# Kernel tuning notes

Hardware: AMD Instinct MI355X
Metric: run time of the kernel (lower is better)

The kernel has to match this reference:

```python
import jax, jax.numpy as jnp
import numpy as np
import math

B, S, E, H = 4, 1024, 1024, 16
D = E // H


def setup_inputs() -> dict:
    key = jax.random.key(0)
    ks = jax.random.split(key, 10)
    inp = {
        "query": jax.random.normal(ks[0], (B, S, E), dtype=jnp.float32),
        "key": jax.random.normal(ks[1], (B, S, E), dtype=jnp.float32),
        "value": jax.random.normal(ks[2], (B, S, E), dtype=jnp.float32),
        "attn_mask": jax.random.randint(ks[3], (B * H, S, S), 0, 2).astype(bool),
        "key_padding_mask": jax.random.randint(ks[4], (B, S), 0, 2).astype(bool),
        # nn.Linear(E, E, bias=False) weights, stored [out, in] as in torch
        "Wq": jax.random.normal(ks[5], (E, E), dtype=jnp.float32) * 0.02,
        "Wk": jax.random.normal(ks[6], (E, E), dtype=jnp.float32) * 0.02,
        "Wv": jax.random.normal(ks[7], (E, E), dtype=jnp.float32) * 0.02,
        "Wo": jax.random.normal(ks[8], (E, E), dtype=jnp.float32) * 0.02,
    }
    return inp


def reference(query, key, value, attn_mask, key_padding_mask, Wq, Wk, Wv, Wo):
    # projections: torch Linear => x @ W.T; split heads -> [B,H,S,D]
    Q = (query @ Wq.T).reshape(B, S, H, D).transpose(0, 2, 1, 3)
    K = (key @ Wk.T).reshape(B, S, H, D).transpose(0, 2, 1, 3)
    V = (value @ Wv.T).reshape(B, S, H, D).transpose(0, 2, 1, 3)

    scores = jnp.einsum('bhid,bhkd->bhik', Q, K) / math.sqrt(D)  # [B,H,S,S]

    am = attn_mask.reshape(B, H, S, S)
    kpm = jnp.broadcast_to(key_padding_mask[:, None, None, :], (B, H, S, S))
    mask = am | kpm

    # faithful quirks: masked scores set to 0 (not -inf); softmax over dim=2
    # (the QUERY axis i of [b,h,i,k]); masked weights zeroed after softmax.
    scores = jnp.where(mask, 0.0, scores)
    weights = jax.nn.softmax(scores, axis=2)
    weights = jnp.where(mask, 0.0, weights)

    attn = jnp.einsum('bhij,bhjk->bhik', weights, V)  # [B,H,S,D]
    attn = attn.transpose(0, 2, 1, 3).reshape(B, S, H * D)
    return attn @ Wo.T
```

## Files before the change

### kernel.cpp

```cpp
#include <hip/hip_runtime.h>
#include <stdint.h>

#define S_ 1024
#define E_ 1024
#define H_ 16
#define D_ 64
#define BH_ 64

typedef __attribute__((ext_vector_type(4))) float f32x4;
typedef __attribute__((ext_vector_type(8))) short bf16x8;

__device__ __forceinline__ ushort f2bf(float f) {
  union { float f; uint32_t u; } c; c.f = f;
  uint32_t u = c.u;
  return (ushort)((u + 0x7FFFu + ((u >> 16) & 1u)) >> 16);
}

__device__ __forceinline__ void gl_lds16(const void* g, void* l) {
  __builtin_amdgcn_global_load_lds((__attribute__((address_space(1))) void*)(g),
                                   (__attribute__((address_space(3))) void*)(l), 16, 0, 0);
}

__global__ __launch_bounds__(256) void cvt_bf16(const float* __restrict__ q,
                                                const float* __restrict__ k,
                                                const float* __restrict__ v,
                                                const float* __restrict__ wq,
                                                const float* __restrict__ wk,
                                                const float* __restrict__ wv,
                                                const float* __restrict__ wo,
                                                ushort* __restrict__ dst) {
  size_t i = ((size_t)blockIdx.x * 256 + threadIdx.x) * 4;
  const size_t M4 = 4u << 20, M1 = 1u << 20;
  const float* src;
  size_t off;
  if (i < M4) { src = q; off = i; }
  else if (i < 2 * M4) { src = k; off = i - M4; }
  else if (i < 3 * M4) { src = v; off = i - 2 * M4; }
  else if (i < 3 * M4 + M1) { src = wq; off = i - 3 * M4; }
  else if (i < 3 * M4 + 2 * M1) { src = wk; off = i - (3 * M4 + M1); }
  else if (i < 3 * M4 + 3 * M1) { src = wv; off = i - (3 * M4 + 2 * M1); }
  else { src = wo; off = i - (3 * M4 + 3 * M1); }
  float4 f = *reinterpret_cast<const float4*>(src + off);
  ushort4 o;
  o.x = f2bf(f.x); o.y = f2bf(f.y); o.z = f2bf(f.z); o.w = f2bf(f.w);
  *reinterpret_cast<ushort4*>(dst + i) = o;
}

__global__ __launch_bounds__(256) void pack_mask(const int* __restrict__ am,
                                                 const int* __restrict__ kpm,
                                                 uint32_t* __restrict__ mw) {
  size_t t = (size_t)blockIdx.x * 256 + threadIdx.x;
  size_t f = t * 4;
  int k = (int)(f & (S_ - 1));
  int b = (int)(f >> 24);
  int4 a = *reinterpret_cast<const int4*>(am + f);
  int4 kp = *reinterpret_cast<const int4*>(kpm + (size_t)b * S_ + k);
  uint32_t nib = (uint32_t)((a.x | kp.x) != 0) | ((uint32_t)((a.y | kp.y) != 0) << 1) |
                 ((uint32_t)((a.z | kp.z) != 0) << 2) | ((uint32_t)((a.w | kp.w) != 0) << 3);
  uint32_t v = nib << ((threadIdx.x & 7) * 4);
  v |= __shfl_xor(v, 1);
  v |= __shfl_xor(v, 2);
  v |= __shfl_xor(v, 4);
  if ((threadIdx.x & 7) == 0) mw[t >> 3] = v;
}

__global__ __launch_bounds__(256) void gemm_proj(const ushort* __restrict__ qkv,
                                                 const ushort* __restrict__ wts,
                                                 ushort* __restrict__ QKo,
                                                 ushort* __restrict__ Vt) {
  const int K = 1024, BM = 128, BK = 32;
  __shared__ ushort As[BM * BK];
  __shared__ ushort Bs[BM * BK];
  const int tid = threadIdx.x, wave = tid >> 6, lane = tid & 63;
  const int l15 = lane & 15, lk = lane >> 4;
  const int wr = wave >> 1, wc = wave & 1;
  const int mb = blockIdx.x, nb = blockIdx.y, z = blockIdx.z;
  const ushort* A = qkv + (size_t)z * (4u << 20);
  const ushort* Bw = wts + (size_t)z * (1u << 20);
  const int srow = (lane >> 2);
  const int scol = (lane & 3) * 8;
  f32x4 acc[4][4] = {};
  for (int kt = 0; kt < K / BK; ++kt) {
#pragma unroll
    for (int c = 0; c < 2; ++c) {
      int ch = wave * 2 + c;
      int row = ch * 16 + srow;
      gl_lds16(&A[(size_t)(mb * BM + row) * K + kt * BK + scol], &As[ch * 512]);
      gl_lds16(&Bw[(size_t)(nb * BM + row) * K + kt * BK + scol], &Bs[ch * 512]);
    }
    __syncthreads();
    bf16x8 a[4], b[4];
#pragma unroll
    for (int m = 0; m < 4; ++m)
      a[m] = *reinterpret_cast<const bf16x8*>(&As[(wr * 64 + m * 16 + l15) * BK + lk * 8]);
#pragma unroll
    for (int n = 0; n < 4; ++n)
      b[n] = *reinterpret_cast<const bf16x8*>(&Bs[(wc * 64 + n * 16 + l15) * BK + lk * 8]);
#pragma unroll
    for (int m = 0; m < 4; ++m)
#pragma unroll
      for (int n = 0; n < 4; ++n)
        acc[m][n] = __builtin_amdgcn_mfma_f32_16x16x32_bf16(a[m], b[n], acc[m][n], 0, 0, 0);
    __syncthreads();
  }
#pragma unroll
  for (int m = 0; m < 4; ++m) {
#pragma unroll
    for (int n = 0; n < 4; ++n) {
#pragma unroll
      for (int r = 0; r < 4; ++r) {
        int gm = mb * BM + wr * 64 + m * 16 + lk * 4 + r;
        int gn = nb * BM + wc * 64 + n * 16 + l15;
        int bb = gm >> 10, s = gm & 1023, h = gn >> 6, d = gn & 63;
        int bh = bb * 16 + h;
        ushort v = f2bf(acc[m][n][r]);
        if (z == 2)
          Vt[((size_t)bh * D_ + d) * S_ + s] = v;
        else
          QKo[(size_t)z * (4u << 20) + ((size_t)bh * S_ + s) * D_ + d] = v;
      }
    }
  }
}

__global__ __launch_bounds__(256) void gemm_out(const ushort* __restrict__ An,
                                                const ushort* __restrict__ Bw,
                                                float* __restrict__ outp) {
  const int K = 1024, BM = 128, BN = 64, BK = 32;
  __shared__ ushort As[BM * BK];
  __shared__ ushort Bs[BN * BK];
  const int tid = threadIdx.x, wave = tid >> 6, lane = tid & 63;
  const int l15 = lane & 15, lk = lane >> 4;
  const int wr = wave >> 1, wc = wave & 1;
  const int mb = blockIdx.x, nb = blockIdx.y;
  const int srow = (lane >> 2), scol = (lane & 3) * 8;
  f32x4 acc[4][2] = {};
  for (int kt = 0; kt < K / BK; ++kt) {
#pragma unroll
    for (int c = 0; c < 2; ++c) {
      int ch = wave * 2 + c;
      int row = ch * 16 + srow;
      gl_lds16(&An[(size_t)(mb * BM + row) * K + kt * BK + scol], &As[ch * 512]);
    }
    {
      int row = wave * 16 + srow;
      gl_lds16(&Bw[(size_t)(nb * BN + row) * K + kt * BK + scol], &Bs[wave * 512]);
    }
    __syncthreads();
    bf16x8 a[4], b[2];
#pragma unroll
    for (int m = 0; m < 4; ++m)
      a[m] = *reinterpret_cast<const bf16x8*>(&As[(wr * 64 + m * 16 + l15) * BK + lk * 8]);
#pragma unroll
    for (int n = 0; n < 2; ++n)
      b[n] = *reinterpret_cast<const bf16x8*>(&Bs[(wc * 32 + n * 16 + l15) * BK + lk * 8]);
#pragma unroll
    for (int m = 0; m < 4; ++m)
#pragma unroll
      for (int n = 0; n < 2; ++n)
        acc[m][n] = __builtin_amdgcn_mfma_f32_16x16x32_bf16(a[m], b[n], acc[m][n], 0, 0, 0);
    __syncthreads();
  }
#pragma unroll
  for (int m = 0; m < 4; ++m) {
#pragma unroll
    for (int n = 0; n < 2; ++n) {
#pragma unroll
      for (int r = 0; r < 4; ++r) {
        int gm = mb * BM + wr * 64 + m * 16 + lk * 4 + r;
        int gn = nb * BN + wc * 32 + n * 16 + l15;
        outp[(size_t)gm * 1024 + gn] = acc[m][n][r];
      }
    }
  }
}

__global__ __launch_bounds__(256) void attn_pass_a(const ushort* __restrict__ Qh,
                                                   const ushort* __restrict__ Kh,
                                                   const uint32_t* __restrict__ mw,
                                                   float* __restrict__ denom) {
  const int TI = 128, TK = 128, LD = 72;
  __shared__ ushort Qs[TI * LD];
  __shared__ ushort Ks[TK * LD];
  __shared__ uint32_t Ms[TI * 4];
  __shared__ float red[4][64];
  const int tid = threadIdx.x, wave = tid >> 6, lane = tid & 63;
  const int l15 = lane & 15, lk = lane >> 4;
  const int wr = wave >> 1, wc = wave & 1;
  const int bh = blockIdx.y, kb = blockIdx.x;
  const ushort* Qb = Qh + (size_t)bh * S_ * D_;
  const ushort* Kb = Kh + (size_t)bh * S_ * D_;
  const uint32_t* mrow = mw + (size_t)bh * S_ * 32;
#pragma unroll
  for (int j = 0; j < 4; ++j) {
    int c = tid + j * 256;
    int row = c >> 3, c8 = c & 7;
    *reinterpret_cast<uint4*>(&Ks[row * LD + c8 * 8]) =
        *reinterpret_cast<const uint4*>(&Kb[(size_t)(kb * TK + row) * D_ + c8 * 8]);
  }
  float csum[4] = {0.f, 0.f, 0.f, 0.f};
  for (int ib = 0; ib < S_ / TI; ++ib) {
    __syncthreads();
#pragma unroll
    for (int j = 0; j < 4; ++j) {
      int c = tid + j * 256;
      int row = c >> 3, c8 = c & 7;
      *reinterpret_cast<uint4*>(&Qs[row * LD + c8 * 8]) =
          *reinterpret_cast<const uint4*>(&Qb[(size_t)(ib * TI + row) * D_ + c8 * 8]);
    }
    if (tid < 512) Ms[tid] = mrow[(size_t)(ib * TI + (tid >> 2)) * 32 + kb * 4 + (tid & 3)];
    __syncthreads();
    f32x4 acc[4][4] = {};
#pragma unroll
    for (int kk = 0; kk < 2; ++kk) {
      bf16x8 a[4], b[4];
#pragma unroll
      for (int m = 0; m < 4; ++m)
        a[m] = *reinterpret_cast<const bf16x8*>(&Qs[(wr * 64 + m * 16 + l15) * LD + kk * 32 + lk * 8]);
#pragma unroll
      for (int n = 0; n < 4; ++n)
        b[n] = *reinterpret_cast<const bf16x8*>(&Ks[(wc * 64 + n * 16 + l15) * LD + kk * 32 + lk * 8]);
#pragma unroll
      for (int m = 0; m < 4; ++m)
#pragma unroll
        for (int n = 0; n < 4; ++n)
          acc[m][n] = __builtin_amdgcn_mfma_f32_16x16x32_bf16(a[m], b[n], acc[m][n], 0, 0, 0);
    }
#pragma unroll
    for (int n = 0; n < 4; ++n) {
      int kwl = wc * 2 + (n >> 1);
      int kbit = (n & 1) * 16 + l15;
      float part = 0.f;
#pragma unroll
      for (int m = 0; m < 4; ++m) {
        int lr0 = wr * 64 + m * 16 + lk * 4;
#pragma unroll
        for (int r = 0; r < 4; ++r) {
          bool msk = (Ms[(lr0 + r) * 4 + kwl] >> kbit) & 1;
          float s = acc[m][n][r] * 0.125f;
          part += msk ? 1.0f : __expf(s);
        }
      }
      csum[n] += part;
    }
  }
#pragma unroll
  for (int n = 0; n < 4; ++n) {
    float v = csum[n];
    v += __shfl_xor(v, 16);
    v += __shfl_xor(v, 32);
    csum[n] = v;
  }
  __syncthreads();
  if (lane < 16) {
#pragma unroll
    for (int n = 0; n < 4; ++n) red[wave][n * 16 + l15] = csum[n];
  }
  __syncthreads();
  if (tid < 128) {
    int wcx = tid >> 6, col = tid & 63;
    denom[(size_t)bh * S_ + kb * TK + wcx * 64 + col] = red[wcx][col] + red[wcx + 2][col];
  }
}

__global__ __launch_bounds__(256) void attn_pass_b(const ushort* __restrict__ Qh,
                                                   const ushort* __restrict__ Kh,
                                                   const ushort* __restrict__ Vt,
                                                   const uint32_t* __restrict__ mw,
                                                   const float* __restrict__ denom,
                                                   ushort* __restrict__ An) {
  const int TI = 128, TK = 64, LD = 72;
  __shared__ ushort Qs[TI * LD];
  __shared__ ushort Ks[TK * LD];
  __shared__ ushort Ws[TI * LD];
  __shared__ uint32_t Ms[TI * 2];
  __shared__ float dinv[TK];
  const int tid = threadIdx.x, wave = tid >> 6, lane = tid & 63;
  const int l15 = lane & 15, lk = lane >> 4;
  const int wr = wave >> 1, wc = wave & 1;
  const int bh = blockIdx.y, ib = blockIdx.x;
  const ushort* Qb = Qh + (size_t)bh * S_ * D_;
  const ushort* Kb = Kh + (size_t)bh * S_ * D_;
  const ushort* Vb = Vt + (size_t)bh * D_ * S_;
  const uint32_t* mrow = mw + (size_t)bh * S_ * 32;
#pragma unroll
  for (int j = 0; j < 4; ++j) {
    int c = tid + j * 256;
    int row = c >> 3, c8 = c & 7;
    *reinterpret_cast<uint4*>(&Qs[row * LD + c8 * 8]) =
        *reinterpret_cast<const uint4*>(&Qb[(size_t)(ib * TI + row) * D_ + c8 * 8]);
  }
  f32x4 acc2[2][4] = {};
  for (int kt = 0; kt < S_ / TK; ++kt) {
    __syncthreads();
#pragma unroll
    for (int j = 0; j < 2; ++j) {
      int c = tid + j * 256;
      int row = c >> 3, c8 = c & 7;
      *reinterpret_cast<uint4*>(&Ks[row * LD + c8 * 8]) =
          *reinterpret_cast<const uint4*>(&Kb[(size_t)(kt * TK + row) * D_ + c8 * 8]);
    }
    if (tid < 256) Ms[tid] = mrow[(size_t)(ib * TI + (tid >> 1)) * 32 + kt * 2 + (tid & 1)];
    if (tid < TK) dinv[tid] = 1.0f / denom[(size_t)bh * S_ + kt * TK + tid];
    __syncthreads();
    f32x4 acc[4][2] = {};
#pragma unroll
    for (int kk = 0; kk < 2; ++kk) {
      bf16x8 a[4], b[2];
#pragma unroll
      for (int m = 0; m < 4; ++m)
        a[m] = *reinterpret_cast<const bf16x8*>(&Qs[(wr * 64 + m * 16 + l15) * LD + kk * 32 + lk * 8]);
#pragma unroll
      for (int n = 0; n < 2; ++n)
        b[n] = *reinterpret_cast<const bf16x8*>(&Ks[(wc * 32 + n * 16 + l15) * LD + kk * 32 + lk * 8]);
#pragma unroll
      for (int m = 0; m < 4; ++m)
#pragma unroll
        for (int n = 0; n < 2; ++n)
          acc[m][n] = __builtin_amdgcn_mfma_f32_16x16x32_bf16(a[m], b[n], acc[m][n], 0, 0, 0);
    }
#pragma unroll
    for (int n = 0; n < 2; ++n) {
      int kcol = wc * 32 + n * 16 + l15;
      int kwl = kcol >> 5;
      int kbit = kcol & 31;
      float di = dinv[kcol];
#pragma unroll
      for (int m = 0; m < 4; ++m) {
        int lrow = wr * 64 + m * 16 + lk * 4;
#pragma unroll
        for (int r = 0; r < 4; ++r) {
          bool msk = (Ms[(lrow + r) * 2 + kwl] >> kbit) & 1;
          float s = acc[m][n][r] * 0.125f;
          float wv = msk ? 0.f : __expf(s) * di;
          Ws[(lrow + r) * LD + kcol] = f2bf(wv);
        }
      }
    }
    __syncthreads();
#pragma unroll
    for (int kk = 0; kk < 2; ++kk) {
      bf16x8 a2[2], b2[4];
#pragma unroll
      for (int m = 0; m < 2; ++m)
        a2[m] = *reinterpret_cast<const bf16x8*>(&Ws[(wave * 32 + m * 16 + l15) * LD + kk * 32 + lk * 8]);
#pragma unroll
      for (int n = 0; n < 4; ++n)
        b2[n] = *reinterpret_cast<const bf16x8*>(&Vb[(size_t)(n * 16 + l15) * S_ + kt * TK + kk * 32 + lk * 8]);
#pragma unroll
      for (int m = 0; m < 2; ++m)
#pragma unroll
        for (int n = 0; n < 4; ++n)
          acc2[m][n] = __builtin_amdgcn_mfma_f32_16x16x32_bf16(a2[m], b2[n], acc2[m][n], 0, 0, 0);
    }
  }
  const int b_ = bh >> 4, h = bh & 15;
#pragma unroll
  for (int m = 0; m < 2; ++m) {
#pragma unroll
    for (int n = 0; n < 4; ++n) {
#pragma unroll
      for (int r = 0; r < 4; ++r) {
        int i = ib * TI + wave * 32 + m * 16 + lk * 4 + r;
        int d = n * 16 + l15;
        An[((size_t)(b_ * S_ + i)) * E_ + h * D_ + d] = f2bf(acc2[m][n][r]);
      }
    }
  }
}

extern "C" void kernel_launch(void* const* d_in, const int* in_sizes, int n_in,
                              void* d_out, int out_size, void* d_ws, size_t ws_size,
                              hipStream_t stream) {
  const float* q = (const float*)d_in[0];
  const float* k = (const float*)d_in[1];
  const float* v = (const float*)d_in[2];
  const int* am = (const int*)d_in[3];
  const int* kpm = (const int*)d_in[4];
  const float* Wq = (const float*)d_in[5];
  const float* Wk = (const float*)d_in[6];
  const float* Wv = (const float*)d_in[7];
  const float* Wo = (const float*)d_in[8];
  float* out = (float*)d_out;

  ushort* cvt = (ushort*)d_ws;
  ushort* qkv = cvt;
  ushort* wts = cvt + (12u << 20);
  ushort* wob = cvt + (15u << 20);
  uint8_t* ws = (uint8_t*)d_ws;
  ushort* Qh = (ushort*)(ws + (32ull << 20));
  ushort* Kh = (ushort*)(ws + (40ull << 20));
  ushort* Vt = (ushort*)(ws + (48ull << 20));
  ushort* An = qkv;
  uint32_t* MW = (uint32_t*)(ws + (56ull << 20));
  float* Dn = (float*)(ws + (64ull << 20));

  cvt_bf16<<<16384, 256, 0, stream>>>(q, k, v, Wq, Wk, Wv, Wo, cvt);
  pack_mask<<<65536, 256, 0, stream>>>(am, kpm, MW);
  gemm_proj<<<dim3(32, 8, 3), 256, 0, stream>>>(qkv, wts, Qh, Vt);
  attn_pass_a<<<dim3(8, 64), 256, 0, stream>>>(Qh, Kh, MW, Dn);
  attn_pass_b<<<dim3(8, 64), 256, 0, stream>>>(Qh, Kh, Vt, MW, Dn, An);
  gemm_out<<<dim3(32, 16), 256, 0, stream>>>(An, wob, out);
}
```

Before: 581.3 us.

## Materialize unnormalized attention weights once, fold denominator into V, switch to fp16

Pass A now computes exp(scores) once, writes the masked unnormalized weights to a global fp16 buffer and accumulates column sums. A new kernel scales V by the reciprocal denominators, and a plain GEMM multiplies the stored weights by the scaled V. This removes the second QK^T and exp recomputation that pass B used to do. The 1/sqrt(D) scale is folded into the Q projection epilogue, and all operands switch from bf16 to fp16 MFMA. The cost is writing and re-reading a 128 MB weight matrix, plus fp16 range and precision risk (e.g. exp overflow, V/denom underflow).

```diff
diff --git a/kernel.cpp b/kernel.cpp
--- a/kernel.cpp
+++ b/kernel.cpp
@@ -8,27 +8,21 @@
 #define BH_ 64
 
 typedef __attribute__((ext_vector_type(4))) float f32x4;
-typedef __attribute__((ext_vector_type(8))) short bf16x8;
-
-__device__ __forceinline__ ushort f2bf(float f) {
-  union { float f; uint32_t u; } c; c.f = f;
-  uint32_t u = c.u;
-  return (ushort)((u + 0x7FFFu + ((u >> 16) & 1u)) >> 16);
-}
+typedef __attribute__((ext_vector_type(8))) _Float16 f16x8;
 
 __device__ __forceinline__ void gl_lds16(const void* g, void* l) {
   __builtin_amdgcn_global_load_lds((__attribute__((address_space(1))) void*)(g),
                                    (__attribute__((address_space(3))) void*)(l), 16, 0, 0);
 }
 
-__global__ __launch_bounds__(256) void cvt_bf16(const float* __restrict__ q,
-                                                const float* __restrict__ k,
-                                                const float* __restrict__ v,
-                                                const float* __restrict__ wq,
-                                                const float* __restrict__ wk,
-                                                const float* __restrict__ wv,
-                                                const float* __restrict__ wo,
-                                                ushort* __restrict__ dst) {
+__global__ __launch_bounds__(256) void cvt_f16(const float* __restrict__ q,
+                                               const float* __restrict__ k,
+                                               const float* __restrict__ v,
+                                               const float* __restrict__ wq,
+                                               const float* __restrict__ wk,
+                                               const float* __restrict__ wv,
+                                               const float* __restrict__ wo,
+                                               _Float16* __restrict__ dst) {
   size_t i = ((size_t)blockIdx.x * 256 + threadIdx.x) * 4;
   const size_t M4 = 4u << 20, M1 = 1u << 20;
   const float* src;
@@ -41,9 +35,9 @@
   else if (i < 3 * M4 + 3 * M1) { src = wv; off = i - (3 * M4 + 2 * M1); }
   else { src = wo; off = i - (3 * M4 + 3 * M1); }
   float4 f = *reinterpret_cast<const float4*>(src + off);
-  ushort4 o;
-  o.x = f2bf(f.x); o.y = f2bf(f.y); o.z = f2bf(f.z); o.w = f2bf(f.w);
-  *reinterpret_cast<ushort4*>(dst + i) = o;
+  _Float16 h[4];
+  h[0] = (_Float16)f.x; h[1] = (_Float16)f.y; h[2] = (_Float16)f.z; h[3] = (_Float16)f.w;
+  *reinterpret_cast<uint2*>(dst + i) = *reinterpret_cast<uint2*>(h);
 }
 
 __global__ __launch_bounds__(256) void pack_mask(const int* __restrict__ am,
@@ -64,19 +58,19 @@
   if ((threadIdx.x & 7) == 0) mw[t >> 3] = v;
 }
 
-__global__ __launch_bounds__(256) void gemm_proj(const ushort* __restrict__ qkv,
-                                                 const ushort* __restrict__ wts,
-                                                 ushort* __restrict__ QKo,
-                                                 ushort* __restrict__ Vt) {
+__global__ __launch_bounds__(256) void gemm_proj(const _Float16* __restrict__ qkv,
+                                                 const _Float16* __restrict__ wts,
+                                                 _Float16* __restrict__ QKo,
+                                                 _Float16* __restrict__ Vt) {
   const int K = 1024, BM = 128, BK = 32;
-  __shared__ ushort As[BM * BK];
-  __shared__ ushort Bs[BM * BK];
+  __shared__ __align__(16) _Float16 As[BM * BK];
+  __shared__ __align__(16) _Float16 Bs[BM * BK];
   const int tid = threadIdx.x, wave = tid >> 6, lane = tid & 63;
   const int l15 = lane & 15, lk = lane >> 4;
   const int wr = wave >> 1, wc = wave & 1;
   const int mb = blockIdx.x, nb = blockIdx.y, z = blockIdx.z;
-  const ushort* A = qkv + (size_t)z * (4u << 20);
-  const ushort* Bw = wts + (size_t)z * (1u << 20);
+  const _Float16* A = qkv + (size_t)z * (4u << 20);
+  const _Float16* Bw = wts + (size_t)z * (1u << 20);
   const int srow = (lane >> 2);
   const int scol = (lane & 3) * 8;
   f32x4 acc[4][4] = {};
@@ -89,20 +83,21 @@
       gl_lds16(&Bw[(size_t)(nb * BM + row) * K + kt * BK + scol], &Bs[ch * 512]);
     }
     __syncthreads();
-    bf16x8 a[4], b[4];
+    f16x8 a[4], b[4];
 #pragma unroll
     for (int m = 0; m < 4; ++m)
-      a[m] = *reinterpret_cast<const bf16x8*>(&As[(wr * 64 + m * 16 + l15) * BK + lk * 8]);
+      a[m] = *reinterpret_cast<const f16x8*>(&As[(wr * 64 + m * 16 + l15) * BK + lk * 8]);
 #pragma unroll
     for (int n = 0; n < 4; ++n)
-      b[n] = *reinterpret_cast<const bf16x8*>(&Bs[(wc * 64 + n * 16 + l15) * BK + lk * 8]);
+      b[n] = *reinterpret_cast<const f16x8*>(&Bs[(wc * 64 + n * 16 + l15) * BK + lk * 8]);
 #pragma unroll
     for (int m = 0; m < 4; ++m)
 #pragma unroll
       for (int n = 0; n < 4; ++n)
-        acc[m][n] = __builtin_amdgcn_mfma_f32_16x16x32_bf16(a[m], b[n], acc[m][n], 0, 0, 0);
-    __syncthreads();
-  }
+        acc[m][n] = __builtin_amdgcn_mfma_f32_16x16x32_f16(a[m], b[n], acc[m][n], 0, 0, 0);
+    __syncthreads();
+  }
+  const float qs = (z == 0) ? 0.125f : 1.0f;
 #pragma unroll
   for (int m = 0; m < 4; ++m) {
 #pragma unroll
@@ -113,7 +108,7 @@
         int gn = nb * BM + wc * 64 + n * 16 + l15;
         int bb = gm >> 10, s = gm & 1023, h = gn >> 6, d = gn & 63;
         int bh = bb * 16 + h;
-        ushort v = f2bf(acc[m][n][r]);
+        _Float16 v = (_Float16)(acc[m][n][r] * qs);
         if (z == 2)
           Vt[((size_t)bh * D_ + d) * S_ + s] = v;
         else
@@ -123,12 +118,194 @@
   }
 }
 
-__global__ __launch_bounds__(256) void gemm_out(const ushort* __restrict__ An,
-                                                const ushort* __restrict__ Bw,
-                                                float* __restrict__ outp) {
+__global__ __launch_bounds__(256) void attn_pass_a(const _Float16* __restrict__ Qh,
+                                                   const _Float16* __restrict__ Kh,
+                                                   const uint32_t* __restrict__ mw,
+                                                   float* __restrict__ denom,
+                                                   _Float16* __restrict__ Wg) {
+  const int TI = 128, TK = 128, LD = 72, LW = 144;
+  __shared__ __align__(16) _Float16 Qs[TI * LD];
+  __shared__ __align__(16) _Float16 Ks[TK * LD];
+  __shared__ __align__(16) _Float16 Ws[TI * LW];
+  __shared__ uint32_t Ms[TI * 4];
+  __shared__ float red[4][64];
+  const int tid = threadIdx.x, wave = tid >> 6, lane = tid & 63;
+  const int l15 = lane & 15, lk = lane >> 4;
+  const int wr = wave >> 1, wc = wave & 1;
+  const int bh = blockIdx.y, kb = blockIdx.x;
+  const _Float16* Qb = Qh + (size_t)bh * S_ * D_;
+  const _Float16* Kb = Kh + (size_t)bh * S_ * D_;
+  const uint32_t* mrow = mw + (size_t)bh * S_ * 32;
+#pragma unroll
+  for (int j = 0; j < 4; ++j) {
+    int c = tid + j * 256;
+    int row = c >> 3, c8 = c & 7;
+    *reinterpret_cast<uint4*>(&Ks[row * LD + c8 * 8]) =
+        *reinterpret_cast<const uint4*>(&Kb[(size_t)(kb * TK + row) * D_ + c8 * 8]);
+  }
+  float csum[4] = {0.f, 0.f, 0.f, 0.f};
+  for (int ib = 0; ib < S_ / TI; ++ib) {
+    __syncthreads();
+#pragma unroll
+    for (int j = 0; j < 4; ++j) {
+      int c = tid + j * 256;
+      int row = c >> 3, c8 = c & 7;
+      *reinterpret_cast<uint4*>(&Qs[row * LD + c8 * 8]) =
+          *reinterpret_cast<const uint4*>(&Qb[(size_t)(ib * TI + row) * D_ + c8 * 8]);
+    }
+    Ms[tid] = mrow[(size_t)(ib * TI + (tid >> 2)) * 32 + kb * 4 + (tid & 3)];
+    Ms[tid + 256] = mrow[(size_t)(ib * TI + 64 + (tid >> 2)) * 32 + kb * 4 + (tid & 3)];
+    __syncthreads();
+    f32x4 acc[4][4] = {};
+#pragma unroll
+    for (int kk = 0; kk < 2; ++kk) {
+      f16x8 a[4], b[4];
+#pragma unroll
+      for (int m = 0; m < 4; ++m)
+        a[m] = *reinterpret_cast<const f16x8*>(&Qs[(wr * 64 + m * 16 + l15) * LD + kk * 32 + lk * 8]);
+#pragma unroll
+      for (int n = 0; n < 4; ++n)
+        b[n] = *reinterpret_cast<const f16x8*>(&Ks[(wc * 64 + n * 16 + l15) * LD + kk * 32 + lk * 8]);
+#pragma unroll
+      for (int m = 0; m < 4; ++m)
+#pragma unroll
+        for (int n = 0; n < 4; ++n)
+          acc[m][n] = __builtin_amdgcn_mfma_f32_16x16x32_f16(a[m], b[n], acc[m][n], 0, 0, 0);
+    }
+#pragma unroll
+    for (int n = 0; n < 4; ++n) {
+      int kcol = wc * 64 + n * 16 + l15;
+      int kwl = kcol >> 5;
+      int kbit = kcol & 31;
+      float part = 0.f;
+#pragma unroll
+      for (int m = 0; m < 4; ++m) {
+        int lr0 = wr * 64 + m * 16 + lk * 4;
+#pragma unroll
+        for (int r = 0; r < 4; ++r) {
+          bool msk = (Ms[(lr0 + r) * 4 + kwl] >> kbit) & 1;
+          float e = __expf(acc[m][n][r]);
+          part += msk ? 1.0f : e;
+          Ws[(lr0 + r) * LW + kcol] = msk ? (_Float16)0.f : (_Float16)e;
+        }
+      }
+      csum[n] += part;
+    }
+    __syncthreads();
+#pragma unroll
+    for (int j = 0; j < 8; ++j) {
+      int c = tid + j * 256;
+      int row = c >> 4, col8 = c & 15;
+      *reinterpret_cast<uint4*>(
+          &Wg[((size_t)bh << 20) + (size_t)(ib * TI + row) * 1024 + kb * TK + col8 * 8]) =
+          *reinterpret_cast<const uint4*>(&Ws[row * LW + col8 * 8]);
+    }
+  }
+#pragma unroll
+  for (int n = 0; n < 4; ++n) {
+    float v = csum[n];
+    v += __shfl_xor(v, 16);
+    v += __shfl_xor(v, 32);
+    csum[n] = v;
+  }
+  __syncthreads();
+  if (lane < 16) {
+#pragma unroll
+    for (int n = 0; n < 4; ++n) red[wave][n * 16 + l15] = csum[n];
+  }
+  __syncthreads();
+  if (tid < 128) {
+    int wcx = tid >> 6, col = tid & 63;
+    denom[(size_t)bh * S_ + kb * TK + wcx * 64 + col] = red[wcx][col] + red[wcx + 2][col];
+  }
+}
+
+__global__ __launch_bounds__(256) void vscale(_Float16* __restrict__ Vt,
+                                              const float* __restrict__ Dn) {
+  size_t e = ((size_t)blockIdx.x * 256 + threadIdx.x) * 8;
+  int bh = (int)(e >> 16);
+  int s = (int)(e & (S_ - 1));
+  uint4 raw = *reinterpret_cast<uint4*>(Vt + e);
+  _Float16* h = reinterpret_cast<_Float16*>(&raw);
+  const float* dp = Dn + (size_t)bh * S_ + s;
+#pragma unroll
+  for (int j = 0; j < 8; ++j) h[j] = (_Float16)((float)h[j] / dp[j]);
+  *reinterpret_cast<uint4*>(Vt + e) = raw;
+}
+
+__global__ __launch_bounds__(256) void gemm_pv(const _Float16* __restrict__ Wg,
+                                               const _Float16* __restrict__ Vp,
+                                               _Float16* __restrict__ An) {
+  const int BK = 64;
+  __shared__ __align__(16) _Float16 As[128 * BK];
+  __shared__ __align__(16) _Float16 Bs[64 * BK];
+  const int tid = threadIdx.x, wave = tid >> 6, lane = tid & 63;
+  const int l15 = lane & 15, lk = lane >> 4;
+  const int wr = wave >> 1, wc = wave & 1;
+  const int ibl = blockIdx.x, bh = blockIdx.y;
+  const _Float16* Wb = Wg + ((size_t)bh << 20) + (size_t)ibl * 128 * 1024;
+  const _Float16* Vb = Vp + ((size_t)bh << 16);
+  f32x4 acc[4][2] = {};
+  for (int kt = 0; kt < 16; ++kt) {
+#pragma unroll
+    for (int j = 0; j < 4; ++j) {
+      int c = tid + j * 256;
+      int row = c >> 3, slot = c & 7;
+      int gs = slot ^ (row & 7);
+      gl_lds16(&Wb[(size_t)row * 1024 + kt * BK + gs * 8], &As[c * 8]);
+    }
+#pragma unroll
+    for (int j = 0; j < 2; ++j) {
+      int c = tid + j * 256;
+      int row = c >> 3, slot = c & 7;
+      int gs = slot ^ (row & 7);
+      gl_lds16(&Vb[(size_t)row * 1024 + kt * BK + gs * 8], &Bs[c * 8]);
+    }
+    __syncthreads();
+#pragma unroll
+    for (int kk = 0; kk < 2; ++kk) {
+      f16x8 a[4], b[2];
+#pragma unroll
+      for (int m = 0; m < 4; ++m) {
+        int row = wr * 64 + m * 16 + l15;
+        int slot = (kk * 4 + lk) ^ (row & 7);
+        a[m] = *reinterpret_cast<const f16x8*>(&As[row * BK + slot * 8]);
+      }
+#pragma unroll
+      for (int n = 0; n < 2; ++n) {
+        int row = wc * 32 + n * 16 + l15;
+        int slot = (kk * 4 + lk) ^ (row & 7);
+        b[n] = *reinterpret_cast<const f16x8*>(&Bs[row * BK + slot * 8]);
+      }
+#pragma unroll
+      for (int m = 0; m < 4; ++m)
+#pragma unroll
+        for (int n = 0; n < 2; ++n)
+          acc[m][n] = __builtin_amdgcn_mfma_f32_16x16x32_f16(a[m], b[n], acc[m][n], 0, 0, 0);
+    }
+    __syncthreads();
+  }
+  const int b_ = bh >> 4, h = bh & 15;
+#pragma unroll
+  for (int m = 0; m < 4; ++m) {
+#pragma unroll
+    for (int n = 0; n < 2; ++n) {
+#pragma unroll
+      for (int r = 0; r < 4; ++r) {
+        int i = ibl * 128 + wr * 64 + m * 16 + lk * 4 + r;
+        int d = wc * 32 + n * 16 + l15;
+        An[((size_t)(b_ * S_ + i)) * E_ + h * D_ + d] = (_Float16)acc[m][n][r];
+      }
+    }
+  }
+}
+
+__global__ __launch_bounds__(256) void gemm_out(const _Float16* __restrict__ An,
+                                               const _Float16* __restrict__ Bw,
+                                               float* __restrict__ outp) {
   const int K = 1024, BM = 128, BN = 64, BK = 32;
-  __shared__ ushort As[BM * BK];
-  __shared__ ushort Bs[BN * BK];
+  __shared__ __align__(16) _Float16 As[BM * BK];
+  __shared__ __align__(16) _Float16 Bs[BN * BK];
   const int tid = threadIdx.x, wave = tid >> 6, lane = tid & 63;
   const int l15 = lane & 15, lk = lane >> 4;
   const int wr = wave >> 1, wc = wave & 1;
@@ -147,18 +324,18 @@
       gl_lds16(&Bw[(size_t)(nb * BN + row) * K + kt * BK + scol], &Bs[wave * 512]);
     }
     __syncthreads();
-    bf16x8 a[4], b[2];
+    f16x8 a[4], b[2];
 #pragma unroll
     for (int m = 0; m < 4; ++m)
-      a[m] = *reinterpret_cast<const bf16x8*>(&As[(wr * 64 + m * 16 + l15) * BK + lk * 8]);
+      a[m] = *reinterpret_cast<const f16x8*>(&As[(wr * 64 + m * 16 + l15) * BK + lk * 8]);
 #pragma unroll
     for (int n = 0; n < 2; ++n)
-      b[n] = *reinterpret_cast<const bf16x8*>(&Bs[(wc * 32 + n * 16 + l15) * BK + lk * 8]);
+      b[n] = *reinterpret_cast<const f16x8*>(&Bs[(wc * 32 + n * 16 + l15) * BK + lk * 8]);
 #pragma unroll
     for (int m = 0; m < 4; ++m)
 #pragma unroll
       for (int n = 0; n < 2; ++n)
-        acc[m][n] = __builtin_amdgcn_mfma_f32_16x16x32_bf16(a[m], b[n], acc[m][n], 0, 0, 0);
+        acc[m][n] = __builtin_amdgcn_mfma_f32_16x16x32_f16(a[m], b[n], acc[m][n], 0, 0, 0);
     __syncthreads();
   }
 #pragma unroll
@@ -170,200 +347,6 @@
         int gm = mb * BM + wr * 64 + m * 16 + lk * 4 + r;
         int gn = nb * BN + wc * 32 + n * 16 + l15;
         outp[(size_t)gm * 1024 + gn] = acc[m][n][r];
-      }
-    }
-  }
-}
-
-__global__ __launch_bounds__(256) void attn_pass_a(const ushort* __restrict__ Qh,
-                                                   const ushort* __restrict__ Kh,
-                                                   const uint32_t* __restrict__ mw,
-                                                   float* __restrict__ denom) {
-  const int TI = 128, TK = 128, LD = 72;
-  __shared__ ushort Qs[TI * LD];
-  __shared__ ushort Ks[TK * LD];
-  __shared__ uint32_t Ms[TI * 4];
-  __shared__ float red[4][64];
-  const int tid = threadIdx.x, wave = tid >> 6, lane = tid & 63;
-  const int l15 = lane & 15, lk = lane >> 4;
-  const int wr = wave >> 1, wc = wave & 1;
-  const int bh = blockIdx.y, kb = blockIdx.x;
-  const ushort* Qb = Qh + (size_t)bh * S_ * D_;
-  const ushort* Kb = Kh + (size_t)bh * S_ * D_;
-  const uint32_t* mrow = mw + (size_t)bh * S_ * 32;
-#pragma unroll
-  for (int j = 0; j < 4; ++j) {
-    int c = tid + j * 256;
-    int row = c >> 3, c8 = c & 7;
-    *reinterpret_cast<uint4*>(&Ks[row * LD + c8 * 8]) =
-        *reinterpret_cast<const uint4*>(&Kb[(size_t)(kb * TK + row) * D_ + c8 * 8]);
-  }
-  float csum[4] = {0.f, 0.f, 0.f, 0.f};
-  for (int ib = 0; ib < S_ / TI; ++ib) {
-    __syncthreads();
-#pragma unroll
-    for (int j = 0; j < 4; ++j) {
-      int c = tid + j * 256;
-      int row = c >> 3, c8 = c & 7;
-      *reinterpret_cast<uint4*>(&Qs[row * LD + c8 * 8]) =
-          *reinterpret_cast<const uint4*>(&Qb[(size_t)(ib * TI + row) * D_ + c8 * 8]);
-    }
-    if (tid < 512) Ms[tid] = mrow[(size_t)(ib * TI + (tid >> 2)) * 32 + kb * 4 + (tid & 3)];
-    __syncthreads();
-    f32x4 acc[4][4] = {};
-#pragma unroll
-    for (int kk = 0; kk < 2; ++kk) {
-      bf16x8 a[4], b[4];
-#pragma unroll
-      for (int m = 0; m < 4; ++m)
-        a[m] = *reinterpret_cast<const bf16x8*>(&Qs[(wr * 64 + m * 16 + l15) * LD + kk * 32 + lk * 8]);
-#pragma unroll
-      for (int n = 0; n < 4; ++n)
-        b[n] = *reinterpret_cast<const bf16x8*>(&Ks[(wc * 64 + n * 16 + l15) * LD + kk * 32 + lk * 8]);
-#pragma unroll
-      for (int m = 0; m < 4; ++m)
-#pragma unroll
-        for (int n = 0; n < 4; ++n)
-          acc[m][n] = __builtin_amdgcn_mfma_f32_16x16x32_bf16(a[m], b[n], acc[m][n], 0, 0, 0);
-    }
-#pragma unroll
-    for (int n = 0; n < 4; ++n) {
-      int kwl = wc * 2 + (n >> 1);
-      int kbit = (n & 1) * 16 + l15;
-      float part = 0.f;
-#pragma unroll
-      for (int m = 0; m < 4; ++m) {
-        int lr0 = wr * 64 + m * 16 + lk * 4;
-#pragma unroll
-        for (int r = 0; r < 4; ++r) {
-          bool msk = (Ms[(lr0 + r) * 4 + kwl] >> kbit) & 1;
-          float s = acc[m][n][r] * 0.125f;
-          part += msk ? 1.0f : __expf(s);
-        }
-      }
-      csum[n] += part;
-    }
-  }
-#pragma unroll
-  for (int n = 0; n < 4; ++n) {
-    float v = csum[n];
-    v += __shfl_xor(v, 16);
-    v += __shfl_xor(v, 32);
-    csum[n] = v;
-  }
-  __syncthreads();
-  if (lane < 16) {
-#pragma unroll
-    for (int n = 0; n < 4; ++n) red[wave][n * 16 + l15] = csum[n];
-  }
-  __syncthreads();
-  if (tid < 128) {
-    int wcx = tid >> 6, col = tid & 63;
-    denom[(size_t)bh * S_ + kb * TK + wcx * 64 + col] = red[wcx][col] + red[wcx + 2][col];
-  }
-}
-
-__global__ __launch_bounds__(256) void attn_pass_b(const ushort* __restrict__ Qh,
-                                                   const ushort* __restrict__ Kh,
-                                                   const ushort* __restrict__ Vt,
-                                                   const uint32_t* __restrict__ mw,
-                                                   const float* __restrict__ denom,
-                                                   ushort* __restrict__ An) {
-  const int TI = 128, TK = 64, LD = 72;
-  __shared__ ushort Qs[TI * LD];
-  __shared__ ushort Ks[TK * LD];
-  __shared__ ushort Ws[TI * LD];
-  __shared__ uint32_t Ms[TI * 2];
-  __shared__ float dinv[TK];
-  const int tid = threadIdx.x, wave = tid >> 6, lane = tid & 63;
-  const int l15 = lane & 15, lk = lane >> 4;
-  const int wr = wave >> 1, wc = wave & 1;
-  const int bh = blockIdx.y, ib = blockIdx.x;
-  const ushort* Qb = Qh + (size_t)bh * S_ * D_;
-  const ushort* Kb = Kh + (size_t)bh * S_ * D_;
-  const ushort* Vb = Vt + (size_t)bh * D_ * S_;
-  const uint32_t* mrow = mw + (size_t)bh * S_ * 32;
-#pragma unroll
-  for (int j = 0; j < 4; ++j) {
-    int c = tid + j * 256;
-    int row = c >> 3, c8 = c & 7;
-    *reinterpret_cast<uint4*>(&Qs[row * LD + c8 * 8]) =
-        *reinterpret_cast<const uint4*>(&Qb[(size_t)(ib * TI + row) * D_ + c8 * 8]);
-  }
-  f32x4 acc2[2][4] = {};
-  for (int kt = 0; kt < S_ / TK; ++kt) {
-    __syncthreads();
-#pragma unroll
-    for (int j = 0; j < 2; ++j) {
-      int c = tid + j * 256;
-      int row = c >> 3, c8 = c & 7;
-      *reinterpret_cast<uint4*>(&Ks[row * LD + c8 * 8]) =
-          *reinterpret_cast<const uint4*>(&Kb[(size_t)(kt * TK + row) * D_ + c8 * 8]);
-    }
-    if (tid < 256) Ms[tid] = mrow[(size_t)(ib * TI + (tid >> 1)) * 32 + kt * 2 + (tid & 1)];
-    if (tid < TK) dinv[tid] = 1.0f / denom[(size_t)bh * S_ + kt * TK + tid];
-    __syncthreads();
-    f32x4 acc[4][2] = {};
-#pragma unroll
-    for (int kk = 0; kk < 2; ++kk) {
-      bf16x8 a[4], b[2];
-#pragma unroll
-      for (int m = 0; m < 4; ++m)
-        a[m] = *reinterpret_cast<const bf16x8*>(&Qs[(wr * 64 + m * 16 + l15) * LD + kk * 32 + lk * 8]);
-#pragma unroll
-      for (int n = 0; n < 2; ++n)
-        b[n] = *reinterpret_cast<const bf16x8*>(&Ks[(wc * 32 + n * 16 + l15) * LD + kk * 32 + lk * 8]);
-#pragma unroll
-      for (int m = 0; m < 4; ++m)
-#pragma unroll
-        for (int n = 0; n < 2; ++n)
-          acc[m][n] = __builtin_amdgcn_mfma_f32_16x16x32_bf16(a[m], b[n], acc[m][n], 0, 0, 0);
-    }
-#pragma unroll
-    for (int n = 0; n < 2; ++n) {
-      int kcol = wc * 32 + n * 16 + l15;
-      int kwl = kcol >> 5;
-      int kbit = kcol & 31;
-      float di = dinv[kcol];
-#pragma unroll
-      for (int m = 0; m < 4; ++m) {
-        int lrow = wr * 64 + m * 16 + lk * 4;
-#pragma unroll
-        for (int r = 0; r < 4; ++r) {
-          bool msk = (Ms[(lrow + r) * 2 + kwl] >> kbit) & 1;
-          float s = acc[m][n][r] * 0.125f;
-          float wv = msk ? 0.f : __expf(s) * di;
-          Ws[(lrow + r) * LD + kcol] = f2bf(wv);
-        }
-      }
-    }
-    __syncthreads();
-#pragma unroll
-    for (int kk = 0; kk < 2; ++kk) {
-      bf16x8 a2[2], b2[4];
-#pragma unroll
-      for (int m = 0; m < 2; ++m)
-        a2[m] = *reinterpret_cast<const bf16x8*>(&Ws[(wave * 32 + m * 16 + l15) * LD + kk * 32 + lk * 8]);
-#pragma unroll
-      for (int n = 0; n < 4; ++n)
-        b2[n] = *reinterpret_cast<const bf16x8*>(&Vb[(size_t)(n * 16 + l15) * S_ + kt * TK + kk * 32 + lk * 8]);
-#pragma unroll
-      for (int m = 0; m < 2; ++m)
-#pragma unroll
-        for (int n = 0; n < 4; ++n)
-          acc2[m][n] = __builtin_amdgcn_mfma_f32_16x16x32_bf16(a2[m], b2[n], acc2[m][n], 0, 0, 0);
-    }
-  }
-  const int b_ = bh >> 4, h = bh & 15;
-#pragma unroll
-  for (int m = 0; m < 2; ++m) {
-#pragma unroll
-    for (int n = 0; n < 4; ++n) {
-#pragma unroll
-      for (int r = 0; r < 4; ++r) {
-        int i = ib * TI + wave * 32 + m * 16 + lk * 4 + r;
-        int d = n * 16 + l15;
-        An[((size_t)(b_ * S_ + i)) * E_ + h * D_ + d] = f2bf(acc2[m][n][r]);
       }
     }
   }
@@ -383,22 +366,24 @@
   const float* Wo = (const float*)d_in[8];
   float* out = (float*)d_out;
 
-  ushort* cvt = (ushort*)d_ws;
-  ushort* qkv = cvt;
-  ushort* wts = cvt + (12u << 20);
-  ushort* wob = cvt + (15u << 20);
+  _Float16* cvt = (_Float16*)d_ws;
+  _Float16* qkv = cvt;
+  _Float16* wts = cvt + (12u << 20);
+  _Float16* wob = cvt + (15u << 20);
   uint8_t* ws = (uint8_t*)d_ws;
-  ushort* Qh = (ushort*)(ws + (32ull << 20));
-  ushort* Kh = (ushort*)(ws + (40ull << 20));
-  ushort* Vt = (ushort*)(ws + (48ull << 20));
-  ushort* An = qkv;
+  _Float16* Qh = (_Float16*)(ws + (32ull << 20));
+  _Float16* Kh = (_Float16*)(ws + (40ull << 20));
+  _Float16* Vt = (_Float16*)(ws + (48ull << 20));
   uint32_t* MW = (uint32_t*)(ws + (56ull << 20));
   float* Dn = (float*)(ws + (64ull << 20));
-
-  cvt_bf16<<<16384, 256, 0, stream>>>(q, k, v, Wq, Wk, Wv, Wo, cvt);
+  _Float16* Wg = (_Float16*)(ws + (80ull << 20));
+  _Float16* An = qkv;
+
+  cvt_f16<<<16384, 256, 0, stream>>>(q, k, v, Wq, Wk, Wv, Wo, cvt);
   pack_mask<<<65536, 256, 0, stream>>>(am, kpm, MW);
   gemm_proj<<<dim3(32, 8, 3), 256, 0, stream>>>(qkv, wts, Qh, Vt);
-  attn_pass_a<<<dim3(8, 64), 256, 0, stream>>>(Qh, Kh, MW, Dn);
-  attn_pass_b<<<dim3(8, 64), 256, 0, stream>>>(Qh, Kh, Vt, MW, Dn, An);
+  attn_pass_a<<<dim3(8, 64), 256, 0, stream>>>(Qh, Kh, MW, Dn, Wg);
+  vscale<<<2048, 256, 0, stream>>>(Vt, Dn);
+  gemm_pv<<<dim3(8, 64), 256, 0, stream>>>(Wg, Vt, An);
   gemm_out<<<dim3(32, 16), 256, 0, stream>>>(An, wob, out);
 }
```

Result: faster. 567.1 us (-2.4%).
